# Performance work log

Measured on AMD Instinct MI355X. Metric: run time of the kernel, lower is better.

## Reference

```python
import jax, jax.numpy as jnp
import numpy as np
from jax import lax

N, L, C_IN, NOISE_C, COMP, NC = 256, 512, 514, 112, 16, 2
MAIN_IN = NOISE_C + COMP  # 128
FEAT = NC * 4 * L         # 4096

def _conv1d(x, w, b, pad):
    # x [N,C,L], w [O,I,K]
    y = lax.conv_general_dilated(x, w, (1,), [(pad, pad)], dimension_numbers=('NCH', 'OIH', 'NCH'))
    return y + b[None, :, None]

def _bn(x, g, b):
    # BatchNorm1d, training mode: biased batch stats over (N, L)
    m = x.mean(axis=(0, 2), keepdims=True)
    v = x.var(axis=(0, 2), keepdims=True)
    return (x - m) * lax.rsqrt(v + 1e-5) * g[None, :, None] + b[None, :, None]

def _lrelu(x):
    return jnp.where(x >= 0, x, 0.2 * x)

def _pos_encode(length, dim):
    j = np.arange(dim)
    div = 1.0 / np.power(10000.0, 2 * (j[:, None] // 2) / dim)   # [dim,1]
    ang = np.arange(length)[None, :] * div                       # [dim,length]
    ang = np.where((j % 2 == 0)[:, None], np.sin(ang), np.cos(ang))
    return jnp.asarray(ang[None], jnp.float32)                   # [1,dim,length]

def _assemble(circle_prob, slider_prob):
    # Vectorized run-length label expansion equivalent to the per-sample python while-loop.
    # circle_prob [N, L/2, 2], slider_prob [N, L/4, 2] -> [N, L, 3]
    n, B = slider_prob.shape[0], slider_prob.shape[1]
    c = jnp.argmax(circle_prob, -1)
    s = jnp.argmax(slider_prob, -1)
    zc = jnp.zeros(circle_prob.shape[:-1] + (1,), circle_prob.dtype)
    zs = jnp.zeros(slider_prob.shape[:-1] + (1,), slider_prob.dtype)
    cp3 = jnp.concatenate([circle_prob, zc], -1)                                   # insert 0 at class 2
    sp3 = jnp.concatenate([slider_prob[..., :1], zs, slider_prob[..., 1:]], -1)    # insert 0 at class 1
    pad100 = jnp.array([1., 0., 0.], cp3.dtype)
    pad001 = jnp.array([0., 0., 1.], cp3.dtype)
    bidx = jnp.arange(B)[None, :]
    # slider-body blocks: slider run continues and not cut by sequence end
    body = (s == 1) & (bidx < B - 1)
    prev_body = jnp.concatenate([jnp.zeros((n, 1), bool), body[:, :-1]], 1)
    # tail block ends a slider run (either run stops, or boundary block)
    tail = ((s == 1) & (bidx == B - 1)) | ((s == 0) & prev_body)
    # circle emission for each half-step: prob row if predicted circle else pad
    cr0 = jnp.where((c == 1)[..., None], cp3, pad100).reshape(n, B, 2, 3)
    bodyE = body[..., None]
    row0 = jnp.where((body | tail)[..., None], sp3, cr0[:, :, 0, :])
    row1 = jnp.where(bodyE, pad001, pad100)
    row2 = jnp.where(bodyE, pad001, cr0[:, :, 1, :])
    row3 = jnp.where(bodyE, pad001, pad100)
    return jnp.stack([row0, row1, row2, row3], 2).reshape(n, 4 * B, 3)

def _forward(noise, cond_data, gumbel_u, ext_w1, ext_b1, ext_w2, ext_b2, ext_bn_g, ext_bn_b,
             m_w1, m_b1, m_w2, m_b2, m_bn_g, m_bn_b, lin_w, lin_b, circ_w, circ_b, slid_w, slid_b):
    # FeatureExtractor
    x = cond_data.transpose(0, 2, 1)                      # [N, 514, L]
    x = _lrelu(_conv1d(x, ext_w1, ext_b1, 0))             # [N, 32, L]
    cond = _bn(_conv1d(x, ext_w2, ext_b2, 1), ext_bn_g, ext_bn_b)  # [N, 16, L]
    gen_in = jnp.concatenate([cond, noise.transpose(0, 2, 1)], 1) + _pos_encode(L, MAIN_IN)  # [N,128,L]
    h = _lrelu(_conv1d(gen_in, m_w1, m_b1, 3))            # [N, 32, L]
    h = _lrelu(_bn(_conv1d(h, m_w2, m_b2, 1), m_bn_g, m_bn_b))     # [N, 8, L]
    flat = _lrelu(h.reshape(h.shape[0], -1) @ lin_w + lin_b)       # [N, 4096]
    circle_prob = (flat @ circ_w + circ_b).reshape(-1, L // 2, NC)
    slider_prob = (flat @ slid_w + slid_b).reshape(-1, L // 4, NC)
    out = _assemble(circle_prob, slider_prob)             # [N, L, 3]
    # gumbel_softmax(hard=True, tau=1)
    g = -jnp.log(-jnp.log(gumbel_u + 1e-10) + 1e-10)
    logits = out + g
    y_soft = jax.nn.softmax(logits, -1)
    y_hard = jax.nn.one_hot(jnp.argmax(logits, -1), 3, dtype=y_soft.dtype)
    gen_out = y_hard + y_soft - lax.stop_gradient(y_soft)
    return gen_out, cond

def setup_inputs() -> dict:
    key = jax.random.key(0)
    ks = jax.random.split(key, 12)
    def rn(k, shape, fan_in):
        return jax.random.normal(k, shape, jnp.float32) * (1.0 / fan_in) ** 0.5
    return {
        'noise': jax.random.normal(ks[0], (N, L, NOISE_C), jnp.float32),
        'cond_data': jax.random.normal(ks[1], (N, L, C_IN), jnp.float32),
        'gumbel_u': jax.random.uniform(ks[2], (N, L, 3), jnp.float32),
        'ext_w1': rn(ks[3], (C_IN // 16, C_IN, 1), C_IN), 'ext_b1': jnp.zeros(C_IN // 16),
        'ext_w2': rn(ks[4], (COMP, C_IN // 16, 3), 3 * (C_IN // 16)), 'ext_b2': jnp.zeros(COMP),
        'ext_bn_g': jnp.ones(COMP), 'ext_bn_b': jnp.zeros(COMP),
        'm_w1': rn(ks[5], (NC * 16, MAIN_IN, 7), 7 * MAIN_IN), 'm_b1': jnp.zeros(NC * 16),
        'm_w2': rn(ks[6], (NC * 4, NC * 16, 3), 3 * NC * 16), 'm_b2': jnp.zeros(NC * 4),
        'm_bn_g': jnp.ones(NC * 4), 'm_bn_b': jnp.zeros(NC * 4),
        'lin_w': rn(ks[7], (FEAT, FEAT), FEAT), 'lin_b': jnp.zeros(FEAT),
        'circ_w': rn(ks[8], (FEAT, NC * L // 2), FEAT), 'circ_b': jnp.zeros(NC * L // 2),
        'slid_w': rn(ks[9], (FEAT, NC * L // 4), FEAT), 'slid_b': jnp.zeros(NC * L // 4),
    }

def reference(noise, cond_data, gumbel_u, ext_w1, ext_b1, ext_w2, ext_b2, ext_bn_g, ext_bn_b,
              m_w1, m_b1, m_w2, m_b2, m_bn_g, m_bn_b, lin_w, lin_b, circ_w, circ_b, slid_w, slid_b):
    return _forward(noise, cond_data, gumbel_u, ext_w1, ext_b1, ext_w2, ext_b2, ext_bn_g, ext_bn_b,
                    m_w1, m_b1, m_w2, m_b2, m_bn_g, m_bn_b, lin_w, lin_b, circ_w, circ_b, slid_w, slid_b)
```

## Files before the change

### kernel.cpp

```cpp
#include <hip/hip_runtime.h>
#include <math.h>

#define NB 256
#define LL 512
#define CIN 514

__device__ __forceinline__ float lrelu(float x) { return x >= 0.f ? x : 0.2f * x; }

__global__ __launch_bounds__(256) void k_pos(float* __restrict__ pos) {
    int idx = blockIdx.x * 256 + threadIdx.x;
    int c = idx >> 9, l = idx & 511;
    double e = (double)(2 * (c >> 1)) / 128.0;
    double dv = 1.0 / pow(10000.0, e);
    double a = (double)l * dv;
    pos[idx] = (float)((c & 1) ? cos(a) : sin(a));
}

__global__ __launch_bounds__(256) void k_conv1(const float* __restrict__ X, const float* __restrict__ W,
                                               const float* __restrict__ bias, float* __restrict__ out) {
    __shared__ __align__(16) float As[32][260];
    __shared__ __align__(16) float Bs[32][32];
    const int t = threadIdx.x;
    const int pos0 = blockIdx.x * 256;
    const int tx = t & 31, ty = t >> 5;
    const int rl = t >> 4, kp = t & 15;
    float acc[8][4];
#pragma unroll
    for (int p = 0; p < 8; ++p)
#pragma unroll
        for (int q = 0; q < 4; ++q) acc[p][q] = 0.f;

    for (int k0 = 0; k0 < CIN; k0 += 32) {
#pragma unroll
        for (int pass = 0; pass < 16; ++pass) {
            int row = pass * 16 + rl;
            int kk = kp * 2, gk = k0 + kk;
            float vx = 0.f, vy = 0.f;
            if (gk + 1 < CIN) {
                float2 v = *reinterpret_cast<const float2*>(X + (size_t)(pos0 + row) * CIN + gk);
                vx = v.x; vy = v.y;
            } else if (gk < CIN) {
                vx = X[(size_t)(pos0 + row) * CIN + gk];
            }
            As[kk][row] = vx;
            As[kk + 1][row] = vy;
        }
        {
            int o = t & 31, kg = t >> 5;
#pragma unroll
            for (int j = 0; j < 4; ++j) {
                int kk = kg * 4 + j, gk = k0 + kk;
                Bs[kk][o] = (gk < CIN) ? W[o * CIN + gk] : 0.f;
            }
        }
        __syncthreads();
#pragma unroll 8
        for (int kk = 0; kk < 32; ++kk) {
            float4 a0 = *reinterpret_cast<const float4*>(&As[kk][tx * 4]);
            float4 a1 = *reinterpret_cast<const float4*>(&As[kk][128 + tx * 4]);
            float4 b  = *reinterpret_cast<const float4*>(&Bs[kk][ty * 4]);
            float av[8] = {a0.x,a0.y,a0.z,a0.w,a1.x,a1.y,a1.z,a1.w};
            float bv[4] = {b.x,b.y,b.z,b.w};
#pragma unroll
            for (int p = 0; p < 8; ++p)
#pragma unroll
                for (int q = 0; q < 4; ++q) acc[p][q] += av[p] * bv[q];
        }
        __syncthreads();
    }
    const int n = pos0 >> 9, l0 = pos0 & 511;
#pragma unroll
    for (int q = 0; q < 4; ++q) {
        int o = ty * 4 + q;
        float bb = bias[o];
#pragma unroll
        for (int h = 0; h < 2; ++h) {
            float4 v;
            v.x = lrelu(acc[h*4+0][q] + bb);
            v.y = lrelu(acc[h*4+1][q] + bb);
            v.z = lrelu(acc[h*4+2][q] + bb);
            v.w = lrelu(acc[h*4+3][q] + bb);
            *reinterpret_cast<float4*>(out + ((size_t)n * 32 + o) * LL + l0 + h * 128 + tx * 4) = v;
        }
    }
}

__global__ __launch_bounds__(256) void k_conv2(const float* __restrict__ X, const float* __restrict__ W,
                                               const float* __restrict__ bias, float* __restrict__ out) {
    __shared__ __align__(16) float Xs[32][264];
    __shared__ __align__(16) float Ws[16][32][4];
    const int t = threadIdx.x;
    const int n = blockIdx.x >> 1, l0 = (blockIdx.x & 1) * 256;
    for (int idx = t; idx < 32 * 258; idx += 256) {
        int i = idx / 258, j = idx % 258;
        int gl = l0 - 1 + j;
        Xs[i][j] = (gl >= 0 && gl < LL) ? X[((size_t)n * 32 + i) * LL + gl] : 0.f;
    }
    for (int idx = t; idx < 1536; idx += 256) {
        int o = idx / 96, r = idx % 96;
        Ws[o][r / 3][r % 3] = W[idx];
    }
    __syncthreads();
    const int tx = t & 31, ty = t >> 5;
    float acc[2][8];
#pragma unroll
    for (int q = 0; q < 2; ++q)
#pragma unroll
        for (int p = 0; p < 8; ++p) acc[q][p] = 0.f;
    for (int i = 0; i < 32; ++i) {
        float4 a0 = *(const float4*)&Xs[i][tx*8];
        float4 a1 = *(const float4*)&Xs[i][tx*8+4];
        float4 a2 = *(const float4*)&Xs[i][tx*8+8];
        float a[12] = {a0.x,a0.y,a0.z,a0.w,a1.x,a1.y,a1.z,a1.w,a2.x,a2.y,a2.z,a2.w};
#pragma unroll
        for (int q = 0; q < 2; ++q) {
            float4 b = *(const float4*)&Ws[ty*2+q][i][0];
#pragma unroll
            for (int p = 0; p < 8; ++p)
                acc[q][p] += a[p]*b.x + a[p+1]*b.y + a[p+2]*b.z;
        }
    }
#pragma unroll
    for (int q = 0; q < 2; ++q) {
        int o = ty*2+q; float bb = bias[o];
#pragma unroll
        for (int h = 0; h < 2; ++h) {
            float4 v;
            v.x = acc[q][h*4+0] + bb; v.y = acc[q][h*4+1] + bb;
            v.z = acc[q][h*4+2] + bb; v.w = acc[q][h*4+3] + bb;
            *(float4*)(out + ((size_t)n*16 + o)*LL + l0 + tx*8 + h*4) = v;
        }
    }
}

__global__ __launch_bounds__(256) void k_redstats(const float* __restrict__ src, int C, float* __restrict__ part) {
    const int ch = blockIdx.x, sl = blockIdx.y, t = threadIdx.x;
    float s = 0.f, q = 0.f;
    for (int i = t; i < 4096; i += 256) {
        int n = sl*8 + (i >> 9), l = i & 511;
        float v = src[((size_t)n*C + ch)*LL + l];
        s += v; q += v*v;
    }
    __shared__ float rs[256], rq[256];
    rs[t] = s; rq[t] = q;
    __syncthreads();
    for (int off = 128; off > 0; off >>= 1) {
        if (t < off) { rs[t] += rs[t+off]; rq[t] += rq[t+off]; }
        __syncthreads();
    }
    if (t == 0) { part[(ch*32+sl)*2] = rs[0]; part[(ch*32+sl)*2+1] = rq[0]; }
}

__global__ void k_bnfinal(const float* __restrict__ part, const float* __restrict__ g,
                          const float* __restrict__ b, int C, float* __restrict__ ss) {
    int ch = threadIdx.x;
    if (ch >= C) return;
    float s = 0.f, q = 0.f;
    for (int j = 0; j < 32; ++j) { s += part[(ch*32 + j)*2]; q += part[(ch*32 + j)*2 + 1]; }
    float mean = s * (1.f/131072.f);
    float var = q * (1.f/131072.f) - mean*mean;
    float sc = g[ch] / sqrtf(var + 1e-5f);
    ss[ch] = sc;
    ss[C + ch] = b[ch] - mean * sc;
}

__global__ __launch_bounds__(256) void k_bnapply(const float* __restrict__ src, const float* __restrict__ ss,
        int C, float* __restrict__ dst, int act, int total4) {
    int i4 = blockIdx.x * 256 + threadIdx.x;
    if (i4 >= total4) return;
    int i = i4 << 2;
    int ch = (i >> 9) % C;
    float sc = ss[ch], sh = ss[C + ch];
    float4 v = reinterpret_cast<const float4*>(src)[i4];
    v.x = v.x*sc + sh; v.y = v.y*sc + sh; v.z = v.z*sc + sh; v.w = v.w*sc + sh;
    if (act) { v.x = lrelu(v.x); v.y = lrelu(v.y); v.z = lrelu(v.z); v.w = lrelu(v.w); }
    reinterpret_cast<float4*>(dst)[i4] = v;
}

__global__ __launch_bounds__(256) void k_mconv1(const float* __restrict__ C16, const float* __restrict__ NZ,
        const float* __restrict__ POS, const float* __restrict__ W, const float* __restrict__ bias,
        float* __restrict__ out) {
    __shared__ __align__(16) float Gs[16][264];
    __shared__ __align__(16) float Ws[32][16][8];
    const int t = threadIdx.x;
    const int n = blockIdx.x >> 1, l0 = (blockIdx.x & 1) * 256;
    const int tx = t & 31, ty = t >> 5;
    float acc[4][8];
#pragma unroll
    for (int q = 0; q < 4; ++q)
#pragma unroll
        for (int p = 0; p < 8; ++p) acc[q][p] = 0.f;

    for (int ct = 0; ct < 8; ++ct) {
        if (ct) __syncthreads();
        if (ct == 0) {
            for (int idx = t; idx < 16*262; idx += 256) {
                int c = idx / 262, j = idx % 262;
                int gl = l0 - 3 + j;
                float v = 0.f;
                if (gl >= 0 && gl < LL) v = C16[((size_t)n*16 + c)*LL + gl] + POS[c*LL + gl];
                Gs[c][j] = v;
            }
        } else {
            int nc0 = ct*16 - 16;
            for (int idx = t; idx < 16*262; idx += 256) {
                int c = idx & 15, j = idx >> 4;
                int gl = l0 - 3 + j;
                float v = 0.f;
                if (gl >= 0 && gl < LL) v = NZ[((size_t)n*LL + gl)*112 + nc0 + c] + POS[(ct*16 + c)*LL + gl];
                Gs[c][j] = v;
            }
        }
        for (int idx = t; idx < 32*112; idx += 256) {
            int o = idx / 112, r = idx % 112;
            Ws[o][r / 7][r % 7] = W[(size_t)o*896 + ct*112 + r];
        }
        __syncthreads();
        for (int ci = 0; ci < 16; ++ci) {
            float4 a0 = *(const float4*)&Gs[ci][tx*8];
            float4 a1 = *(const float4*)&Gs[ci][tx*8+4];
            float4 a2 = *(const float4*)&Gs[ci][tx*8+8];
            float4 a3 = *(const float4*)&Gs[ci][tx*8+12];
            float a[16] = {a0.x,a0.y,a0.z,a0.w,a1.x,a1.y,a1.z,a1.w,
                           a2.x,a2.y,a2.z,a2.w,a3.x,a3.y,a3.z,a3.w};
#pragma unroll
            for (int q = 0; q < 4; ++q) {
                float4 b0 = *(const float4*)&Ws[ty*4+q][ci][0];
                float4 b1 = *(const float4*)&Ws[ty*4+q][ci][4];
                float b[7] = {b0.x,b0.y,b0.z,b0.w,b1.x,b1.y,b1.z};
#pragma unroll
                for (int p = 0; p < 8; ++p) {
#pragma unroll
                    for (int k = 0; k < 7; ++k) acc[q][p] += a[p+k]*b[k];
                }
            }
        }
    }
#pragma unroll
    for (int q = 0; q < 4; ++q) {
        int o = ty*4 + q;
        float bb = bias[o];
#pragma unroll
        for (int h = 0; h < 2; ++h) {
            float4 v;
            v.x = lrelu(acc[q][h*4+0] + bb);
            v.y = lrelu(acc[q][h*4+1] + bb);
            v.z = lrelu(acc[q][h*4+2] + bb);
            v.w = lrelu(acc[q][h*4+3] + bb);
            *(float4*)(out + ((size_t)n*32 + o)*LL + l0 + tx*8 + h*4) = v;
        }
    }
}

__global__ __launch_bounds__(256) void k_mconv2(const float* __restrict__ X, const float* __restrict__ W,
        const float* __restrict__ bias, float* __restrict__ out) {
    __shared__ __align__(16) float Xs[32][264];
    __shared__ __align__(16) float Ws[8][32][4];
    const int t = threadIdx.x;
    const int n = blockIdx.x >> 1, l0 = (blockIdx.x & 1) * 256;
    for (int idx = t; idx < 32 * 258; idx += 256) {
        int i = idx / 258, j = idx % 258;
        int gl = l0 - 1 + j;
        Xs[i][j] = (gl >= 0 && gl < LL) ? X[((size_t)n * 32 + i) * LL + gl] : 0.f;
    }
    for (int idx = t; idx < 768; idx += 256) {
        int o = idx / 96, r = idx % 96;
        Ws[o][r / 3][r % 3] = W[idx];
    }
    __syncthreads();
    const int tx = t & 31, ty = t >> 5;
    float acc[8];
#pragma unroll
    for (int p = 0; p < 8; ++p) acc[p] = 0.f;
    for (int i = 0; i < 32; ++i) {
        float4 a0 = *(const float4*)&Xs[i][tx*8];
        float4 a1 = *(const float4*)&Xs[i][tx*8+4];
        float4 a2 = *(const float4*)&Xs[i][tx*8+8];
        float a[12] = {a0.x,a0.y,a0.z,a0.w,a1.x,a1.y,a1.z,a1.w,a2.x,a2.y,a2.z,a2.w};
        float4 b = *(const float4*)&Ws[ty][i][0];
#pragma unroll
        for (int p = 0; p < 8; ++p)
            acc[p] += a[p]*b.x + a[p+1]*b.y + a[p+2]*b.z;
    }
    float bb = bias[ty];
#pragma unroll
    for (int h = 0; h < 2; ++h) {
        float4 v;
        v.x = acc[h*4+0] + bb; v.y = acc[h*4+1] + bb;
        v.z = acc[h*4+2] + bb; v.w = acc[h*4+3] + bb;
        *(float4*)(out + ((size_t)n*8 + ty)*LL + l0 + tx*8 + h*4) = v;
    }
}

__global__ __launch_bounds__(256) void k_lin(const float* __restrict__ A, const float* __restrict__ B,
                                             float* __restrict__ part) {
    __shared__ __align__(16) float As[32][36];
    __shared__ __align__(16) float Bs[32][132];
    const int t = threadIdx.x;
    const int m0 = blockIdx.x * 32, f0 = blockIdx.y * 128, z = blockIdx.z;
    const int tm = t & 7, tf = t >> 3;
    const int mi = t >> 3, kq = t & 7;
    float acc[4][4];
#pragma unroll
    for (int pm = 0; pm < 4; ++pm)
#pragma unroll
        for (int pf = 0; pf < 4; ++pf) acc[pm][pf] = 0.f;
    for (int k0 = z * 2048; k0 < z * 2048 + 2048; k0 += 32) {
        float4 av = *(const float4*)(A + (size_t)(m0 + mi) * 4096 + k0 + kq * 4);
        As[kq*4+0][mi] = av.x; As[kq*4+1][mi] = av.y; As[kq*4+2][mi] = av.z; As[kq*4+3][mi] = av.w;
#pragma unroll
        for (int pass = 0; pass < 4; ++pass) {
            int fi = pass * 32 + kq * 4;
            *(float4*)&Bs[mi][fi] = *(const float4*)(B + (size_t)(k0 + mi) * 4096 + f0 + fi);
        }
        __syncthreads();
#pragma unroll 8
        for (int kk = 0; kk < 32; ++kk) {
            float4 a = *(const float4*)&As[kk][tm * 4];
            float4 b = *(const float4*)&Bs[kk][tf * 4];
            float avv[4] = {a.x,a.y,a.z,a.w};
            float bvv[4] = {b.x,b.y,b.z,b.w};
#pragma unroll
            for (int pm = 0; pm < 4; ++pm)
#pragma unroll
                for (int pf = 0; pf < 4; ++pf) acc[pm][pf] += avv[pm]*bvv[pf];
        }
        __syncthreads();
    }
#pragma unroll
    for (int pm = 0; pm < 4; ++pm) {
        float4 v = {acc[pm][0], acc[pm][1], acc[pm][2], acc[pm][3]};
        *(float4*)(part + ((size_t)z * 256 + m0 + tm * 4 + pm) * 4096 + f0 + tf * 4) = v;
    }
}

__global__ __launch_bounds__(256) void k_linred(const float* __restrict__ part, const float* __restrict__ bias,
        float* __restrict__ out) {
    int i4 = blockIdx.x*256 + threadIdx.x;
    int i = i4 << 2;
    int f = i & 4095;
    float4 a = ((const float4*)part)[i4];
    float4 c = ((const float4*)(part + 1048576))[i4];
    float4 bb = *(const float4*)(bias + f);
    float4 r;
    r.x = lrelu(a.x + c.x + bb.x);
    r.y = lrelu(a.y + c.y + bb.y);
    r.z = lrelu(a.z + c.z + bb.z);
    r.w = lrelu(a.w + c.w + bb.w);
    ((float4*)out)[i4] = r;
}

__global__ __launch_bounds__(256) void k_heads(const float* __restrict__ A, const float* __restrict__ CW,
        const float* __restrict__ SW, float* __restrict__ part) {
    __shared__ __align__(16) float As[32][36];
    __shared__ __align__(16) float Bs[32][132];
    const int t = threadIdx.x;
    const int m0 = blockIdx.x * 32, f0 = blockIdx.y * 128, z = blockIdx.z;
    const float* B; int ldb, fb;
    if (f0 < 512) { B = CW; ldb = 512; fb = f0; } else { B = SW; ldb = 256; fb = f0 - 512; }
    const int tm = t & 7, tf = t >> 3;
    const int mi = t >> 3, kq = t & 7;
    float acc[4][4];
#pragma unroll
    for (int pm = 0; pm < 4; ++pm)
#pragma unroll
        for (int pf = 0; pf < 4; ++pf) acc[pm][pf] = 0.f;
    for (int k0 = z * 512; k0 < z * 512 + 512; k0 += 32) {
        float4 av = *(const float4*)(A + (size_t)(m0 + mi) * 4096 + k0 + kq * 4);
        As[kq*4+0][mi] = av.x; As[kq*4+1][mi] = av.y; As[kq*4+2][mi] = av.z; As[kq*4+3][mi] = av.w;
#pragma unroll
        for (int pass = 0; pass < 4; ++pass) {
            int fi = pass * 32 + kq * 4;
            *(float4*)&Bs[mi][fi] = *(const float4*)(B + (size_t)(k0 + mi) * ldb + fb + fi);
        }
        __syncthreads();
#pragma unroll 8
        for (int kk = 0; kk < 32; ++kk) {
            float4 a = *(const float4*)&As[kk][tm * 4];
            float4 b = *(const float4*)&Bs[kk][tf * 4];
            float avv[4] = {a.x,a.y,a.z,a.w};
            float bvv[4] = {b.x,b.y,b.z,b.w};
#pragma unroll
            for (int pm = 0; pm < 4; ++pm)
#pragma unroll
                for (int pf = 0; pf < 4; ++pf) acc[pm][pf] += avv[pm]*bvv[pf];
        }
        __syncthreads();
    }
#pragma unroll
    for (int pm = 0; pm < 4; ++pm) {
        float4 v = {acc[pm][0], acc[pm][1], acc[pm][2], acc[pm][3]};
        *(float4*)(part + ((size_t)z * 256 + m0 + tm * 4 + pm) * 768 + f0 + tf * 4) = v;
    }
}

__global__ __launch_bounds__(256) void k_headred(const float* __restrict__ part, const float* __restrict__ cb,
        const float* __restrict__ sb, float* __restrict__ circ, float* __restrict__ slid) {
    int i4 = blockIdx.x * 256 + threadIdx.x;
    int i = i4 << 2;
    int n = i / 768, f = i % 768;
    float4 s = {0.f,0.f,0.f,0.f};
#pragma unroll
    for (int ks = 0; ks < 8; ++ks) {
        float4 p = *(const float4*)(part + ((size_t)ks*256 + n)*768 + f);
        s.x += p.x; s.y += p.y; s.z += p.z; s.w += p.w;
    }
    if (f < 512) {
        float4 bb = *(const float4*)(cb + f);
        s.x += bb.x; s.y += bb.y; s.z += bb.z; s.w += bb.w;
        *(float4*)(circ + (size_t)n*512 + f) = s;
    } else {
        float4 bb = *(const float4*)(sb + f - 512);
        s.x += bb.x; s.y += bb.y; s.z += bb.z; s.w += bb.w;
        *(float4*)(slid + (size_t)n*256 + f - 512) = s;
    }
}

__global__ __launch_bounds__(128) void k_assemble(const float* __restrict__ circ, const float* __restrict__ slid,
        const float* __restrict__ gum, float* __restrict__ out) {
    const int n = blockIdx.x;
    const int b = threadIdx.x;
    const float* sp = slid + (size_t)n * 256;
    const float* cp = circ + (size_t)n * 512;
    float sl0 = sp[2*b], sl1 = sp[2*b+1];
    int s = sl1 > sl0 ? 1 : 0;
    int prevb = 0;
    if (b > 0) prevb = (sp[2*b-1] > sp[2*b-2]) ? 1 : 0;
    bool body = (s == 1) && (b < 127);
    bool tail = ((s == 1) && (b == 127)) || ((s == 0) && (prevb == 1));
    float c0a = cp[4*b], c0b = cp[4*b+1], c1a = cp[4*b+2], c1b = cp[4*b+3];
    bool cA = c0b > c0a, cB = c1b > c1a;
    float rows[4][3];
    if (body || tail)      { rows[0][0]=sl0; rows[0][1]=0.f; rows[0][2]=sl1; }
    else if (cA)           { rows[0][0]=c0a; rows[0][1]=c0b; rows[0][2]=0.f; }
    else                   { rows[0][0]=1.f; rows[0][1]=0.f; rows[0][2]=0.f; }
    if (body)              { rows[1][0]=0.f; rows[1][1]=0.f; rows[1][2]=1.f; }
    else                   { rows[1][0]=1.f; rows[1][1]=0.f; rows[1][2]=0.f; }
    if (body)              { rows[2][0]=0.f; rows[2][1]=0.f; rows[2][2]=1.f; }
    else if (cB)           { rows[2][0]=c1a; rows[2][1]=c1b; rows[2][2]=0.f; }
    else                   { rows[2][0]=1.f; rows[2][1]=0.f; rows[2][2]=0.f; }
    rows[3][0]=rows[1][0]; rows[3][1]=rows[1][1]; rows[3][2]=rows[1][2];
#pragma unroll
    for (int r = 0; r < 4; ++r) {
        int l = 4*b + r;
        const float* u = gum + ((size_t)n*512 + l)*3;
        float g0 = -logf(-logf(u[0]+1e-10f)+1e-10f);
        float g1 = -logf(-logf(u[1]+1e-10f)+1e-10f);
        float g2 = -logf(-logf(u[2]+1e-10f)+1e-10f);
        float t0 = rows[r][0]+g0, t1 = rows[r][1]+g1, t2 = rows[r][2]+g2;
        int am = 0; float mv = t0;
        if (t1 > mv) { am = 1; mv = t1; }
        if (t2 > mv) { am = 2; mv = t2; }
        float e0 = expf(t0-mv), e1 = expf(t1-mv), e2 = expf(t2-mv);
        float ssum = e0+e1+e2;
        float y0 = e0/ssum, y1 = e1/ssum, y2 = e2/ssum;
        float* o = out + ((size_t)n*512 + l)*3;
        o[0] = ((am==0?1.f:0.f) + y0) - y0;
        o[1] = ((am==1?1.f:0.f) + y1) - y1;
        o[2] = ((am==2?1.f:0.f) + y2) - y2;
    }
}

extern "C" void kernel_launch(void* const* d_in, const int* in_sizes, int n_in,
                              void* d_out, int out_size, void* d_ws, size_t ws_size,
                              hipStream_t stream) {
    const float* noise   = (const float*)d_in[0];
    const float* cond    = (const float*)d_in[1];
    const float* gumbel  = (const float*)d_in[2];
    const float* ext_w1  = (const float*)d_in[3];
    const float* ext_b1  = (const float*)d_in[4];
    const float* ext_w2  = (const float*)d_in[5];
    const float* ext_b2  = (const float*)d_in[6];
    const float* ext_bng = (const float*)d_in[7];
    const float* ext_bnb = (const float*)d_in[8];
    const float* m_w1    = (const float*)d_in[9];
    const float* m_b1    = (const float*)d_in[10];
    const float* m_w2    = (const float*)d_in[11];
    const float* m_b2    = (const float*)d_in[12];
    const float* m_bng   = (const float*)d_in[13];
    const float* m_bnb   = (const float*)d_in[14];
    const float* lin_w   = (const float*)d_in[15];
    const float* lin_b   = (const float*)d_in[16];
    const float* circ_w  = (const float*)d_in[17];
    const float* circ_b  = (const float*)d_in[18];
    const float* slid_w  = (const float*)d_in[19];
    const float* slid_b  = (const float*)d_in[20];

    float* genout  = (float*)d_out;
    float* condout = (float*)d_out + 256*512*3;

    float* w     = (float*)d_ws;
    float* x1    = w;
    float* y2    = x1 + 4194304;
    float* posb  = y2 + 2097152;
    float* circ  = posb + 65536;
    float* slid  = circ + 131072;
    float* flatB = slid + 65536;
    float* partL = flatB + 1048576;
    float* partH = partL + 2097152;
    float* stats = partH + 1572864;

    k_pos<<<256, 256, 0, stream>>>(posb);
    k_conv1<<<512, 256, 0, stream>>>(cond, ext_w1, ext_b1, x1);
    k_conv2<<<512, 256, 0, stream>>>(x1, ext_w2, ext_b2, y2);
    k_redstats<<<dim3(16,32), 256, 0, stream>>>(y2, 16, stats);
    k_bnfinal<<<1, 64, 0, stream>>>(stats, ext_bng, ext_bnb, 16, stats + 2048);
    k_bnapply<<<2048, 256, 0, stream>>>(y2, stats + 2048, 16, condout, 0, 524288);
    k_mconv1<<<512, 256, 0, stream>>>(condout, noise, posb, m_w1, m_b1, x1);
    k_mconv2<<<512, 256, 0, stream>>>(x1, m_w2, m_b2, y2);
    k_redstats<<<dim3(8,32), 256, 0, stream>>>(y2, 8, stats);
    k_bnfinal<<<1, 64, 0, stream>>>(stats, m_bng, m_bnb, 8, stats + 2048 + 64);
    k_bnapply<<<1024, 256, 0, stream>>>(y2, stats + 2048 + 64, 8, y2, 1, 262144);
    k_lin<<<dim3(8,32,2), 256, 0, stream>>>(y2, lin_w, partL);
    k_linred<<<1024, 256, 0, stream>>>(partL, lin_b, flatB);
    k_heads<<<dim3(8,6,8), 256, 0, stream>>>(flatB, circ_w, slid_w, partH);
    k_headred<<<192, 256, 0, stream>>>(partH, circ_b, slid_b, circ, slid);
    k_assemble<<<256, 128, 0, stream>>>(circ, slid, gumbel, genout);
}
```

Measured before the change: 610.6 us.

## Split mconv1 input channels across two blocks and precompute positional-encoding conv

The first main conv now splits its 128 input channels into two halves handled by separate blocks, doubling the grid. Each half writes a partial sum, and the second conv adds the two partials and applies the LeakyReLU while loading its tile. Because convolution is linear and the positional encoding is the same for every sample, its contribution (plus bias) is computed once by a new small kernel and added in the epilogue, so the per-element POS loads are gone. Thread-to-position mapping also changes to interleaved 4-wide chunks. The cost is an extra partial buffer that must be written and read back, and one extra launch.

```diff
diff --git a/kernel.cpp b/kernel.cpp
--- a/kernel.cpp
+++ b/kernel.cpp
@@ -14,6 +14,34 @@
     double dv = 1.0 / pow(10000.0, e);
     double a = (double)l * dv;
     pos[idx] = (float)((c & 1) ? cos(a) : sin(a));
+}
+
+__global__ __launch_bounds__(256) void k_posconv(const float* __restrict__ POS, const float* __restrict__ W,
+                                                 const float* __restrict__ bias, float* __restrict__ PC) {
+    const int t = threadIdx.x;
+    const int o = blockIdx.x >> 4, l0 = (blockIdx.x & 15) * 32;
+    const int l = l0 + (t & 31), cs = t >> 5;
+    float acc = 0.f;
+    for (int ci = 0; ci < 16; ++ci) {
+        int c = cs * 16 + ci;
+        float wv[7];
+#pragma unroll
+        for (int k = 0; k < 7; ++k) wv[k] = W[o * 896 + c * 7 + k];
+#pragma unroll
+        for (int k = 0; k < 7; ++k) {
+            int gl = l + k - 3;
+            if (gl >= 0 && gl < LL) acc += wv[k] * POS[c * LL + gl];
+        }
+    }
+    __shared__ float red[8][33];
+    red[cs][t & 31] = acc;
+    __syncthreads();
+    if (cs == 0) {
+        float s = bias[o];
+#pragma unroll
+        for (int j = 0; j < 8; ++j) s += red[j][t & 31];
+        PC[o * LL + l0 + (t & 31)] = s;
+    }
 }
 
 __global__ __launch_bounds__(256) void k_conv1(const float* __restrict__ X, const float* __restrict__ W,
@@ -178,12 +206,12 @@
 }
 
 __global__ __launch_bounds__(256) void k_mconv1(const float* __restrict__ C16, const float* __restrict__ NZ,
-        const float* __restrict__ POS, const float* __restrict__ W, const float* __restrict__ bias,
-        float* __restrict__ out) {
+        const float* __restrict__ PC, const float* __restrict__ W,
+        float* __restrict__ out0, float* __restrict__ out1) {
     __shared__ __align__(16) float Gs[16][264];
     __shared__ __align__(16) float Ws[32][16][8];
     const int t = threadIdx.x;
-    const int n = blockIdx.x >> 1, l0 = (blockIdx.x & 1) * 256;
+    const int n = blockIdx.x >> 2, l0 = ((blockIdx.x >> 1) & 1) * 256, z = blockIdx.x & 1;
     const int tx = t & 31, ty = t >> 5;
     float acc[4][8];
 #pragma unroll
@@ -191,69 +219,75 @@
 #pragma unroll
         for (int p = 0; p < 8; ++p) acc[q][p] = 0.f;
 
-    for (int ct = 0; ct < 8; ++ct) {
-        if (ct) __syncthreads();
-        if (ct == 0) {
+    for (int cc = 0; cc < 4; ++cc) {
+        const int ctg = z * 4 + cc;
+        if (cc) __syncthreads();
+        if (ctg == 0) {
             for (int idx = t; idx < 16*262; idx += 256) {
-                int c = idx / 262, j = idx % 262;
+                int c = idx / 262, j = idx - c * 262;
                 int gl = l0 - 3 + j;
                 float v = 0.f;
-                if (gl >= 0 && gl < LL) v = C16[((size_t)n*16 + c)*LL + gl] + POS[c*LL + gl];
+                if (gl >= 0 && gl < LL) v = C16[((size_t)n*16 + c)*LL + gl];
                 Gs[c][j] = v;
             }
         } else {
-            int nc0 = ct*16 - 16;
+            int nc0 = ctg * 16 - 16;
             for (int idx = t; idx < 16*262; idx += 256) {
                 int c = idx & 15, j = idx >> 4;
                 int gl = l0 - 3 + j;
                 float v = 0.f;
-                if (gl >= 0 && gl < LL) v = NZ[((size_t)n*LL + gl)*112 + nc0 + c] + POS[(ct*16 + c)*LL + gl];
+                if (gl >= 0 && gl < LL) v = NZ[((size_t)n*LL + gl)*112 + nc0 + c];
                 Gs[c][j] = v;
             }
         }
         for (int idx = t; idx < 32*112; idx += 256) {
             int o = idx / 112, r = idx % 112;
-            Ws[o][r / 7][r % 7] = W[(size_t)o*896 + ct*112 + r];
+            Ws[o][r / 7][r % 7] = W[(size_t)o*896 + ctg*112 + r];
         }
         __syncthreads();
         for (int ci = 0; ci < 16; ++ci) {
-            float4 a0 = *(const float4*)&Gs[ci][tx*8];
-            float4 a1 = *(const float4*)&Gs[ci][tx*8+4];
-            float4 a2 = *(const float4*)&Gs[ci][tx*8+8];
-            float4 a3 = *(const float4*)&Gs[ci][tx*8+12];
-            float a[16] = {a0.x,a0.y,a0.z,a0.w,a1.x,a1.y,a1.z,a1.w,
-                           a2.x,a2.y,a2.z,a2.w,a3.x,a3.y,a3.z,a3.w};
+            float4 a0 = *(const float4*)&Gs[ci][tx*4];
+            float4 a1 = *(const float4*)&Gs[ci][tx*4+4];
+            float4 a2 = *(const float4*)&Gs[ci][tx*4+8];
+            float4 a3 = *(const float4*)&Gs[ci][128+tx*4];
+            float4 a4 = *(const float4*)&Gs[ci][128+tx*4+4];
+            float4 a5 = *(const float4*)&Gs[ci][128+tx*4+8];
+            float aA[12] = {a0.x,a0.y,a0.z,a0.w,a1.x,a1.y,a1.z,a1.w,a2.x,a2.y,a2.z,a2.w};
+            float aB[12] = {a3.x,a3.y,a3.z,a3.w,a4.x,a4.y,a4.z,a4.w,a5.x,a5.y,a5.z,a5.w};
 #pragma unroll
             for (int q = 0; q < 4; ++q) {
                 float4 b0 = *(const float4*)&Ws[ty*4+q][ci][0];
                 float4 b1 = *(const float4*)&Ws[ty*4+q][ci][4];
                 float b[7] = {b0.x,b0.y,b0.z,b0.w,b1.x,b1.y,b1.z};
 #pragma unroll
-                for (int p = 0; p < 8; ++p) {
-#pragma unroll
-                    for (int k = 0; k < 7; ++k) acc[q][p] += a[p+k]*b[k];
+                for (int p = 0; p < 4; ++p) {
+#pragma unroll
+                    for (int k = 0; k < 7; ++k) {
+                        acc[q][p]   += aA[p+k]*b[k];
+                        acc[q][4+p] += aB[p+k]*b[k];
+                    }
                 }
             }
         }
     }
+    float* out = z ? out1 : out0;
 #pragma unroll
     for (int q = 0; q < 4; ++q) {
         int o = ty*4 + q;
-        float bb = bias[o];
-#pragma unroll
-        for (int h = 0; h < 2; ++h) {
-            float4 v;
-            v.x = lrelu(acc[q][h*4+0] + bb);
-            v.y = lrelu(acc[q][h*4+1] + bb);
-            v.z = lrelu(acc[q][h*4+2] + bb);
-            v.w = lrelu(acc[q][h*4+3] + bb);
-            *(float4*)(out + ((size_t)n*32 + o)*LL + l0 + tx*8 + h*4) = v;
-        }
-    }
-}
-
-__global__ __launch_bounds__(256) void k_mconv2(const float* __restrict__ X, const float* __restrict__ W,
-        const float* __restrict__ bias, float* __restrict__ out) {
+        float4 p0 = {0.f,0.f,0.f,0.f}, p1 = {0.f,0.f,0.f,0.f};
+        if (z == 0) {
+            p0 = *(const float4*)(PC + o*LL + l0 + tx*4);
+            p1 = *(const float4*)(PC + o*LL + l0 + 128 + tx*4);
+        }
+        float4 v0 = {acc[q][0]+p0.x, acc[q][1]+p0.y, acc[q][2]+p0.z, acc[q][3]+p0.w};
+        float4 v1 = {acc[q][4]+p1.x, acc[q][5]+p1.y, acc[q][6]+p1.z, acc[q][7]+p1.w};
+        *(float4*)(out + ((size_t)n*32 + o)*LL + l0 + tx*4) = v0;
+        *(float4*)(out + ((size_t)n*32 + o)*LL + l0 + 128 + tx*4) = v1;
+    }
+}
+
+__global__ __launch_bounds__(256) void k_mconv2(const float* __restrict__ P0, const float* __restrict__ P1,
+        const float* __restrict__ W, const float* __restrict__ bias, float* __restrict__ out) {
     __shared__ __align__(16) float Xs[32][264];
     __shared__ __align__(16) float Ws[8][32][4];
     const int t = threadIdx.x;
@@ -261,7 +295,12 @@
     for (int idx = t; idx < 32 * 258; idx += 256) {
         int i = idx / 258, j = idx % 258;
         int gl = l0 - 1 + j;
-        Xs[i][j] = (gl >= 0 && gl < LL) ? X[((size_t)n * 32 + i) * LL + gl] : 0.f;
+        float v = 0.f;
+        if (gl >= 0 && gl < LL) {
+            size_t off = ((size_t)n * 32 + i) * LL + gl;
+            v = lrelu(P0[off] + P1[off]);
+        }
+        Xs[i][j] = v;
     }
     for (int idx = t; idx < 768; idx += 256) {
         int o = idx / 96, r = idx % 96;
@@ -499,15 +538,18 @@
     float* partL = flatB + 1048576;
     float* partH = partL + 2097152;
     float* stats = partH + 1572864;
+    float* pc    = stats + 4096;
+    float* buf1  = flatB;
 
     k_pos<<<256, 256, 0, stream>>>(posb);
+    k_posconv<<<512, 256, 0, stream>>>(posb, m_w1, m_b1, pc);
     k_conv1<<<512, 256, 0, stream>>>(cond, ext_w1, ext_b1, x1);
     k_conv2<<<512, 256, 0, stream>>>(x1, ext_w2, ext_b2, y2);
     k_redstats<<<dim3(16,32), 256, 0, stream>>>(y2, 16, stats);
     k_bnfinal<<<1, 64, 0, stream>>>(stats, ext_bng, ext_bnb, 16, stats + 2048);
     k_bnapply<<<2048, 256, 0, stream>>>(y2, stats + 2048, 16, condout, 0, 524288);
-    k_mconv1<<<512, 256, 0, stream>>>(condout, noise, posb, m_w1, m_b1, x1);
-    k_mconv2<<<512, 256, 0, stream>>>(x1, m_w2, m_b2, y2);
+    k_mconv1<<<1024, 256, 0, stream>>>(condout, noise, pc, m_w1, x1, buf1);
+    k_mconv2<<<512, 256, 0, stream>>>(x1, buf1, m_w2, m_b2, y2);
     k_redstats<<<dim3(8,32), 256, 0, stream>>>(y2, 8, stats);
     k_bnfinal<<<1, 64, 0, stream>>>(stats, m_bng, m_bnb, 8, stats + 2048 + 64);
     k_bnapply<<<1024, 256, 0, stream>>>(y2, stats + 2048 + 64, 8, y2, 1, 262144);
```

Result: faster. 588.1 us (-3.7%).
